# Optimization experiments

Measured on AMD Instinct MI355X. Metric: run time of the kernel, lower is better.

The kernel has to match this reference:

```python
import jax, jax.numpy as jnp
import numpy as np

NUM_FIELDS = 64


def setup_inputs() -> dict:
    key = jax.random.key(0)
    x = jax.random.normal(key, (16384, NUM_FIELDS, 128), dtype=jnp.float32)
    return {"x": x}


def reference(x) -> jnp.ndarray:
    # x: [B, F, D]. Pairwise dot products = gram matrix, then upper triangle (i<j).
    gram = jnp.einsum('bfd,bgd->bfg', x, x)  # [B, F, F]
    F = x.shape[1]
    iu, ju = jnp.triu_indices(F, k=1)
    # Row-major (i, j>i) order matches the torch double loop exactly.
    return gram[:, iu, ju]  # [B, F*(F-1)//2]
```

## Files before the change

kernel.cpp:

```cpp
#include <hip/hip_runtime.h>
#include <stdint.h>

#define NF 64
#define ND 128
#define NPAIR 2016
#define THREADS 256

typedef __attribute__((ext_vector_type(4))) float  f32x4;
typedef __attribute__((ext_vector_type(16))) float f32x16;
typedef __attribute__((ext_vector_type(4))) short  s16x4;
typedef __attribute__((ext_vector_type(8))) short  s16x8;

__device__ __forceinline__ short f2bf(float v) {
    union { float f; unsigned u; } c; c.f = v;
    unsigned u = c.u;
    u += 0x7fffu + ((u >> 16) & 1u);
    return (short)(u >> 16);
}

__global__ __launch_bounds__(THREADS, 8) void dotint_kernel(
    const float* __restrict__ x, float* __restrict__ out)
{
    __shared__ short lds[NF * ND];

    const int t = threadIdx.x;
    const long long b = blockIdx.x;

    const f32x4* xg = (const f32x4*)x + b * (NF * ND / 4);
    #pragma unroll
    for (int o = 0; o < 2; ++o) {
        f32x4 v[4];
        #pragma unroll
        for (int i = 0; i < 4; ++i)
            v[i] = xg[t + THREADS * (o * 4 + i)];
        #pragma unroll
        for (int i = 0; i < 4; ++i) {
            const int f     = t + THREADS * (o * 4 + i);
            const int row   = f >> 5;
            const int k4    = f & 31;
            const int kc    = k4 >> 1;
            const int half  = k4 & 1;
            const int chunk = row * 16 + (kc ^ (row & 15));
            s16x4 p;
            p[0] = f2bf(v[i][0]);
            p[1] = f2bf(v[i][1]);
            p[2] = f2bf(v[i][2]);
            p[3] = f2bf(v[i][3]);
            *(s16x4*)&lds[chunk * 8 + half * 4] = p;
        }
    }
    __syncthreads();

    const int wave = t >> 6;
    if (wave < 3) {
        const int lane = t & 63;
        const int lr   = lane & 31;
        const int lh   = lane >> 5;
        const int I = wave >> 1;
        const int J = (wave + 1) >> 1;

        f32x16 acc;
        #pragma unroll
        for (int r = 0; r < 16; ++r) acc[r] = 0.0f;

        #pragma unroll
        for (int kb = 0; kb < 8; ++kb) {
            const int sw = (kb * 2 + lh) ^ (lr & 15);
            s16x8 a = *(const s16x8*)&lds[((I * 32 + lr) * 16 + sw) * 8];
            s16x8 bb = (I == J) ? a
                     : *(const s16x8*)&lds[((J * 32 + lr) * 16 + sw) * 8];
            acc = __builtin_amdgcn_mfma_f32_32x32x16_bf16(a, bb, acc, 0, 0, 0);
        }

        const long long ob = b * (long long)NPAIR;
        #pragma unroll
        for (int r = 0; r < 16; ++r) {
            const int rowInTile = (r & 3) + 8 * (r >> 2) + 4 * lh;
            const int i = I * 32 + rowInTile;
            const int j = J * 32 + lr;
            if (j > i) {
                const int tri = i * (127 - i) / 2 + (j - i - 1);
                out[ob + tri] = acc[r];
            }
        }
    }
}

extern "C" void kernel_launch(void* const* d_in, const int* in_sizes, int n_in,
                              void* d_out, int out_size, void* d_ws, size_t ws_size,
                              hipStream_t stream) {
    const float* x = (const float*)d_in[0];
    float* out = (float*)d_out;
    const int B = in_sizes[0] / (NF * ND);
    dim3 grid(B), block(THREADS);
    hipLaunchKernelGGL(dotint_kernel, grid, block, 0, stream, x, out);
}
```

Baseline: 707.3 us.

## Process multiple batches per block with double-buffered LDS prefetch

Each block now handles eight batch elements and keeps two LDS buffers. While MFMA tiles run on the current element, the next element's fp32 data is loaded into registers, converted to bf16 and written to the other buffer. This is meant to hide global load latency behind compute and cut per-block launch overhead. In exchange the grid shrinks to B/8 blocks (2048), LDS use doubles, and the launch-bounds occupancy hint drops from 8 to 4, which may reduce latency hiding across waves.

```diff
diff --git a/kernel.cpp b/kernel.cpp
--- a/kernel.cpp
+++ b/kernel.cpp
@@ -5,6 +5,7 @@
 #define ND 128
 #define NPAIR 2016
 #define THREADS 256
+#define NB 8
 
 typedef __attribute__((ext_vector_type(4))) float  f32x4;
 typedef __attribute__((ext_vector_type(16))) float f32x16;
@@ -18,71 +19,97 @@
     return (short)(u >> 16);
 }
 
-__global__ __launch_bounds__(THREADS, 8) void dotint_kernel(
-    const float* __restrict__ x, float* __restrict__ out)
+__global__ __launch_bounds__(THREADS, 4) void dotint_kernel(
+    const float* __restrict__ x, float* __restrict__ out, int nbatch)
 {
-    __shared__ short lds[NF * ND];
+    __shared__ short lds[2][NF * ND];
 
     const int t = threadIdx.x;
-    const long long b = blockIdx.x;
+    const long long b0 = (long long)blockIdx.x * NB;
 
-    const f32x4* xg = (const f32x4*)x + b * (NF * ND / 4);
+    const int wave = t >> 6;
+    const int lane = t & 63;
+    const int lr   = lane & 31;
+    const int lh   = lane >> 5;
+    const int I = wave >> 1;
+    const int J = (wave + 1) >> 1;
+
+    int soff[8];
     #pragma unroll
-    for (int o = 0; o < 2; ++o) {
-        f32x4 v[4];
+    for (int k = 0; k < 8; ++k) {
+        const int f    = t + THREADS * k;
+        const int row  = f >> 5;
+        const int k4   = f & 31;
+        const int kc   = k4 >> 1;
+        const int half = k4 & 1;
+        soff[k] = (row * 16 + (kc ^ (row & 15))) * 8 + half * 4;
+    }
+
+    {
+        const f32x4* xg = (const f32x4*)x + b0 * (NF * ND / 4);
+        f32x4 v[8];
         #pragma unroll
-        for (int i = 0; i < 4; ++i)
-            v[i] = xg[t + THREADS * (o * 4 + i)];
+        for (int k = 0; k < 8; ++k) v[k] = xg[t + THREADS * k];
         #pragma unroll
-        for (int i = 0; i < 4; ++i) {
-            const int f     = t + THREADS * (o * 4 + i);
-            const int row   = f >> 5;
-            const int k4    = f & 31;
-            const int kc    = k4 >> 1;
-            const int half  = k4 & 1;
-            const int chunk = row * 16 + (kc ^ (row & 15));
+        for (int k = 0; k < 8; ++k) {
             s16x4 p;
-            p[0] = f2bf(v[i][0]);
-            p[1] = f2bf(v[i][1]);
-            p[2] = f2bf(v[i][2]);
-            p[3] = f2bf(v[i][3]);
-            *(s16x4*)&lds[chunk * 8 + half * 4] = p;
+            p[0] = f2bf(v[k][0]); p[1] = f2bf(v[k][1]);
+            p[2] = f2bf(v[k][2]); p[3] = f2bf(v[k][3]);
+            *(s16x4*)&lds[0][soff[k]] = p;
         }
     }
     __syncthreads();
 
-    const int wave = t >> 6;
-    if (wave < 3) {
-        const int lane = t & 63;
-        const int lr   = lane & 31;
-        const int lh   = lane >> 5;
-        const int I = wave >> 1;
-        const int J = (wave + 1) >> 1;
+    #pragma unroll 2
+    for (int i = 0; i < NB; ++i) {
+        const int cur = i & 1;
+        const long long g = b0 + i;
+        const bool pre = (i + 1 < NB) && (g + 1 < (long long)nbatch);
 
-        f32x16 acc;
-        #pragma unroll
-        for (int r = 0; r < 16; ++r) acc[r] = 0.0f;
-
-        #pragma unroll
-        for (int kb = 0; kb < 8; ++kb) {
-            const int sw = (kb * 2 + lh) ^ (lr & 15);
-            s16x8 a = *(const s16x8*)&lds[((I * 32 + lr) * 16 + sw) * 8];
-            s16x8 bb = (I == J) ? a
-                     : *(const s16x8*)&lds[((J * 32 + lr) * 16 + sw) * 8];
-            acc = __builtin_amdgcn_mfma_f32_32x32x16_bf16(a, bb, acc, 0, 0, 0);
+        f32x4 v[8];
+        if (pre) {
+            const f32x4* xg = (const f32x4*)x + (g + 1) * (NF * ND / 4);
+            #pragma unroll
+            for (int k = 0; k < 8; ++k) v[k] = xg[t + THREADS * k];
         }
 
-        const long long ob = b * (long long)NPAIR;
-        #pragma unroll
-        for (int r = 0; r < 16; ++r) {
-            const int rowInTile = (r & 3) + 8 * (r >> 2) + 4 * lh;
-            const int i = I * 32 + rowInTile;
-            const int j = J * 32 + lr;
-            if (j > i) {
-                const int tri = i * (127 - i) / 2 + (j - i - 1);
-                out[ob + tri] = acc[r];
+        if (wave < 3 && g < (long long)nbatch) {
+            f32x16 acc;
+            #pragma unroll
+            for (int r = 0; r < 16; ++r) acc[r] = 0.0f;
+
+            #pragma unroll
+            for (int kb = 0; kb < 8; ++kb) {
+                const int sw = (kb * 2 + lh) ^ (lr & 15);
+                s16x8 a  = *(const s16x8*)&lds[cur][((I * 32 + lr) * 16 + sw) * 8];
+                s16x8 bb = (I == J) ? a
+                         : *(const s16x8*)&lds[cur][((J * 32 + lr) * 16 + sw) * 8];
+                acc = __builtin_amdgcn_mfma_f32_32x32x16_bf16(a, bb, acc, 0, 0, 0);
+            }
+
+            const long long ob = g * (long long)NPAIR;
+            #pragma unroll
+            for (int r = 0; r < 16; ++r) {
+                const int rowInTile = (r & 3) + 8 * (r >> 2) + 4 * lh;
+                const int ii = I * 32 + rowInTile;
+                const int jj = J * 32 + lr;
+                if (jj > ii) {
+                    const int tri = ii * (127 - ii) / 2 + (jj - ii - 1);
+                    out[ob + tri] = acc[r];
+                }
             }
         }
+
+        if (pre) {
+            #pragma unroll
+            for (int k = 0; k < 8; ++k) {
+                s16x4 p;
+                p[0] = f2bf(v[k][0]); p[1] = f2bf(v[k][1]);
+                p[2] = f2bf(v[k][2]); p[3] = f2bf(v[k][3]);
+                *(s16x4*)&lds[cur ^ 1][soff[k]] = p;
+            }
+        }
+        __syncthreads();
     }
 }
 
@@ -92,6 +119,7 @@
     const float* x = (const float*)d_in[0];
     float* out = (float*)d_out;
     const int B = in_sizes[0] / (NF * ND);
-    dim3 grid(B), block(THREADS);
-    hipLaunchKernelGGL(dotint_kernel, grid, block, 0, stream, x, out);
+    const int grid = (B + NB - 1) / NB;
+    dim3 g(grid), blk(THREADS);
+    hipLaunchKernelGGL(dotint_kernel, g, blk, 0, stream, x, out, B);
 }
```

New measurement: 723.5 us. 1.02x slower.

## Give each wave its own batch, loading fragments from global directly

Applied to the files above, without the earlier changes.

Each wave now handles one whole batch element. It reads fp32 rows straight from global memory into MFMA fragment registers with a one-step register prefetch and computes all three 32x32 gram tiles. This removes the LDS staging, the block barrier and the one idle wave per block. In exchange, the global loads are strided per lane and likely less coalesced than before, and each wave carries more accumulator registers.

```diff
diff --git a/kernel.cpp b/kernel.cpp
--- a/kernel.cpp
+++ b/kernel.cpp
@@ -5,10 +5,10 @@
 #define ND 128
 #define NPAIR 2016
 #define THREADS 256
+#define WPB 4
 
 typedef __attribute__((ext_vector_type(4))) float  f32x4;
 typedef __attribute__((ext_vector_type(16))) float f32x16;
-typedef __attribute__((ext_vector_type(4))) short  s16x4;
 typedef __attribute__((ext_vector_type(8))) short  s16x8;
 
 __device__ __forceinline__ short f2bf(float v) {
@@ -18,69 +18,80 @@
     return (short)(u >> 16);
 }
 
-__global__ __launch_bounds__(THREADS, 8) void dotint_kernel(
-    const float* __restrict__ x, float* __restrict__ out)
+__global__ __launch_bounds__(THREADS, 4) void dotint_kernel(
+    const float* __restrict__ x, float* __restrict__ out, int nbatch)
 {
-    __shared__ short lds[NF * ND];
+    const int t    = threadIdx.x;
+    const int wave = t >> 6;
+    const int lane = t & 63;
+    const int lr   = lane & 31;
+    const int lh   = lane >> 5;
 
-    const int t = threadIdx.x;
-    const long long b = blockIdx.x;
+    const long long g = (long long)blockIdx.x * WPB + wave;
+    if (g >= (long long)nbatch) return;
 
-    const f32x4* xg = (const f32x4*)x + b * (NF * ND / 4);
+    const float* xb = x + g * (NF * ND);
+    const float* p0 = xb + lr * ND + lh * 8;
+    const float* p1 = p0 + 32 * ND;
+
+    f32x16 acc00, acc01, acc11;
     #pragma unroll
-    for (int o = 0; o < 2; ++o) {
-        f32x4 v[4];
-        #pragma unroll
-        for (int i = 0; i < 4; ++i)
-            v[i] = xg[t + THREADS * (o * 4 + i)];
-        #pragma unroll
-        for (int i = 0; i < 4; ++i) {
-            const int f     = t + THREADS * (o * 4 + i);
-            const int row   = f >> 5;
-            const int k4    = f & 31;
-            const int kc    = k4 >> 1;
-            const int half  = k4 & 1;
-            const int chunk = row * 16 + (kc ^ (row & 15));
-            s16x4 p;
-            p[0] = f2bf(v[i][0]);
-            p[1] = f2bf(v[i][1]);
-            p[2] = f2bf(v[i][2]);
-            p[3] = f2bf(v[i][3]);
-            *(s16x4*)&lds[chunk * 8 + half * 4] = p;
-        }
-    }
-    __syncthreads();
+    for (int r = 0; r < 16; ++r) { acc00[r] = 0.f; acc01[r] = 0.f; acc11[r] = 0.f; }
 
-    const int wave = t >> 6;
-    if (wave < 3) {
-        const int lane = t & 63;
-        const int lr   = lane & 31;
-        const int lh   = lane >> 5;
-        const int I = wave >> 1;
-        const int J = (wave + 1) >> 1;
+    f32x4 a0lo = *(const f32x4*)(p0 + 0);
+    f32x4 a0hi = *(const f32x4*)(p0 + 4);
+    f32x4 a1lo = *(const f32x4*)(p1 + 0);
+    f32x4 a1hi = *(const f32x4*)(p1 + 4);
 
-        f32x16 acc;
-        #pragma unroll
-        for (int r = 0; r < 16; ++r) acc[r] = 0.0f;
-
-        #pragma unroll
-        for (int kb = 0; kb < 8; ++kb) {
-            const int sw = (kb * 2 + lh) ^ (lr & 15);
-            s16x8 a = *(const s16x8*)&lds[((I * 32 + lr) * 16 + sw) * 8];
-            s16x8 bb = (I == J) ? a
-                     : *(const s16x8*)&lds[((J * 32 + lr) * 16 + sw) * 8];
-            acc = __builtin_amdgcn_mfma_f32_32x32x16_bf16(a, bb, acc, 0, 0, 0);
+    #pragma unroll
+    for (int kb = 0; kb < 8; ++kb) {
+        f32x4 n0lo, n0hi, n1lo, n1hi;
+        if (kb < 7) {
+            const int ko = (kb + 1) * 16;
+            n0lo = *(const f32x4*)(p0 + ko);
+            n0hi = *(const f32x4*)(p0 + ko + 4);
+            n1lo = *(const f32x4*)(p1 + ko);
+            n1hi = *(const f32x4*)(p1 + ko + 4);
         }
 
-        const long long ob = b * (long long)NPAIR;
+        s16x8 f0, f1;
         #pragma unroll
-        for (int r = 0; r < 16; ++r) {
-            const int rowInTile = (r & 3) + 8 * (r >> 2) + 4 * lh;
-            const int i = I * 32 + rowInTile;
-            const int j = J * 32 + lr;
-            if (j > i) {
-                const int tri = i * (127 - i) / 2 + (j - i - 1);
-                out[ob + tri] = acc[r];
+        for (int e = 0; e < 4; ++e) {
+            f0[e]     = f2bf(a0lo[e]);
+            f0[e + 4] = f2bf(a0hi[e]);
+            f1[e]     = f2bf(a1lo[e]);
+            f1[e + 4] = f2bf(a1hi[e]);
+        }
+
+        acc00 = __builtin_amdgcn_mfma_f32_32x32x16_bf16(f0, f0, acc00, 0, 0, 0);
+        acc01 = __builtin_amdgcn_mfma_f32_32x32x16_bf16(f0, f1, acc01, 0, 0, 0);
+        acc11 = __builtin_amdgcn_mfma_f32_32x32x16_bf16(f1, f1, acc11, 0, 0, 0);
+
+        a0lo = n0lo; a0hi = n0hi; a1lo = n1lo; a1hi = n1hi;
+    }
+
+    const long long ob = g * (long long)NPAIR;
+
+    #pragma unroll
+    for (int r = 0; r < 16; ++r) {
+        const int rowInTile = (r & 3) + 8 * (r >> 2) + 4 * lh;
+        {
+            const int ii = rowInTile, jj = lr;
+            if (jj > ii) {
+                const int tri = ii * (127 - ii) / 2 + (jj - ii - 1);
+                out[ob + tri] = acc00[r];
+            }
+        }
+        {
+            const int ii = rowInTile, jj = 32 + lr;
+            const int tri = ii * (127 - ii) / 2 + (jj - ii - 1);
+            out[ob + tri] = acc01[r];
+        }
+        {
+            const int ii = 32 + rowInTile, jj = 32 + lr;
+            if (jj > ii) {
+                const int tri = ii * (127 - ii) / 2 + (jj - ii - 1);
+                out[ob + tri] = acc11[r];
             }
         }
     }
@@ -92,6 +103,7 @@
     const float* x = (const float*)d_in[0];
     float* out = (float*)d_out;
     const int B = in_sizes[0] / (NF * ND);
-    dim3 grid(B), block(THREADS);
-    hipLaunchKernelGGL(dotint_kernel, grid, block, 0, stream, x, out);
+    const int grid = (B + WPB - 1) / WPB;
+    dim3 g(grid), blk(THREADS);
+    hipLaunchKernelGGL(dotint_kernel, g, blk, 0, stream, x, out, B);
 }
```

Result: slower. 746.5 us (+5.5%).
